# Kernel tuning notes

Hardware: AMD Instinct MI355X
Metric: run time of the kernel (lower is better)

The kernel has to match this reference:

```python
import jax, jax.numpy as jnp
import numpy as np

B, S, NB = 8, 512, 23
INIT, E, R, T = 512, 256, 3, 2
NEG = -9e8

def _gru(x, h, wih, whh, bih, bhh):
    gi = x @ wih.T + bih
    gh = h @ whh.T + bhh
    ir, iz, inn = jnp.split(gi, 3, axis=-1)
    hr, hz, hn = jnp.split(gh, 3, axis=-1)
    r = jax.nn.sigmoid(ir + hr)
    z = jax.nn.sigmoid(iz + hz)
    n = jnp.tanh(inn + r * hn)
    return (1.0 - z) * n + z * h

def setup_inputs():
    key = jax.random.key(0)
    ks = jax.random.split(key, 30)
    def lin(k, o, i):
        return jax.random.normal(k, (o, i), jnp.float32) * 0.02
    def vec(k, n):
        return jax.random.normal(k, (n,), jnp.float32) * 0.02
    inp = {}
    inp["amino_list"] = jax.random.normal(ks[0], (B, S, INIT), jnp.float32)
    inp["amino_mask"] = (jax.random.uniform(ks[1], (B, S)) < 0.9).astype(jnp.float32)
    inp["emb_W"] = lin(ks[2], E, INIT); inp["emb_b"] = vec(ks[3], E)
    inp["nb_W"] = lin(ks[4], E, INIT); inp["nb_b"] = vec(ks[5], E)
    inp["align_W"] = jax.random.normal(ks[6], (R, 1, 2 * E), jnp.float32) * 0.02
    inp["align_b"] = jax.random.normal(ks[7], (R, 1), jnp.float32) * 0.02
    inp["attend_W"] = jax.random.normal(ks[8], (R, E, E), jnp.float32) * 0.02
    inp["attend_b"] = jax.random.normal(ks[9], (R, E), jnp.float32) * 0.02
    inp["gru_wih"] = jax.random.normal(ks[10], (R, 3 * E, E), jnp.float32) * 0.02
    inp["gru_whh"] = jax.random.normal(ks[11], (R, 3 * E, E), jnp.float32) * 0.02
    inp["gru_bih"] = jax.random.normal(ks[12], (R, 3 * E), jnp.float32) * 0.02
    inp["gru_bhh"] = jax.random.normal(ks[13], (R, 3 * E), jnp.float32) * 0.02
    inp["seq_align_W"] = lin(ks[14], 1, 2 * E); inp["seq_align_b"] = vec(ks[15], 1)
    inp["seq_attend_W"] = lin(ks[16], E, E); inp["seq_attend_b"] = vec(ks[17], E)
    inp["seq_gru_wih"] = lin(ks[18], 3 * E, E); inp["seq_gru_bih"] = vec(ks[19], 3 * E)
    inp["seq_gru_whh"] = lin(ks[20], 3 * E, E); inp["seq_gru_bhh"] = vec(ks[21], 3 * E)
    inp["amino_degree_list"] = jax.random.randint(ks[22], (B, S, NB), -1, S)
    return inp

def reference(amino_list, amino_mask, emb_W, emb_b, nb_W, nb_b, align_W, align_b,
              attend_W, attend_b, gru_wih, gru_whh, gru_bih, gru_bhh,
              seq_align_W, seq_align_b, seq_attend_W, seq_attend_b,
              seq_gru_wih, seq_gru_whh, seq_gru_bih, seq_gru_bhh, amino_degree_list):
    idx = amino_degree_list
    lrelu = jax.nn.leaky_relu
    # per-batch neighbor gather: (S,D),(S,NB) -> (S,NB,D); index -1 wraps (masked out below)
    gather = jax.vmap(lambda f, i: f[i])
    feat = lrelu(amino_list @ emb_W.T + emb_b)               # (B,S,E)
    nfeat = lrelu(gather(amino_list, idx) @ nb_W.T + nb_b)   # (B,S,NB,E)
    attend_mask = (idx != -1).astype(feat.dtype)             # (B,S,NB)
    smask = jnp.where(idx == -1, NEG, 0.0).astype(feat.dtype)

    def attn(d, center, nbr):
        # align Linear on concat([center, nbr]) split into two matvecs (same math, no concat)
        aW = align_W[d, 0]
        score = lrelu(jnp.einsum('bse,e->bs', center, aW[:E])[:, :, None]
                      + jnp.einsum('bsne,e->bsn', nbr, aW[E:]) + align_b[d, 0])
        w = jax.nn.softmax(score + smask, axis=-1) * attend_mask   # softmax over neighbor axis
        nt = nbr @ attend_W[d].T + attend_b[d]
        return jax.nn.elu(jnp.einsum('bsn,bsne->bse', w, nt))

    h = _gru(attn(0, feat, nfeat).reshape(-1, E), feat.reshape(-1, E),
             gru_wih[0], gru_whh[0], gru_bih[0], gru_bhh[0])
    act = jax.nn.relu(h.reshape(B, S, E))
    for d in range(1, R):
        ctx = attn(d, act, gather(act, idx))
        h = _gru(ctx.reshape(-1, E), h, gru_wih[d], gru_whh[d], gru_bih[d], gru_bhh[d])
        act = jax.nn.relu(h.reshape(B, S, E))

    seq_feature = jnp.sum(act * amino_mask[:, :, None], axis=1)  # (B,E)
    act_mol = jax.nn.relu(seq_feature)                           # fixed across T (as in torch)
    seq_smask = jnp.where(amino_mask == 0, NEG, 0.0)
    saW = seq_align_W[0]
    act_seq = act_mol
    for _ in range(T):
        score = lrelu((act_mol @ saW[:E])[:, None]
                      + jnp.einsum('bse,e->bs', act, saW[E:]) + seq_align_b[0])
        w = jax.nn.softmax(score + seq_smask, axis=-1) * amino_mask  # softmax over seq axis
        tf = act @ seq_attend_W.T + seq_attend_b
        seq_ctx = jax.nn.elu(jnp.einsum('bs,bse->be', w, tf))
        seq_feature = _gru(seq_ctx, seq_feature, seq_gru_wih, seq_gru_whh, seq_gru_bih, seq_gru_bhh)
        act_seq = jax.nn.relu(seq_feature)
    return (act_seq, act)
```

## Files before the change

kernel.cpp:

```cpp
#include <hip/hip_runtime.h>
#include <math.h>


#define BSZ   8
#define SEQ   512
#define NBR   23
#define EMB   256
#define INITD 512
#define BS    (BSZ*SEQ)
#define G3    (3*EMB)
#define NEGV  -9e8f

typedef __attribute__((ext_vector_type(8))) short short8;
typedef __attribute__((ext_vector_type(4))) float f32x4;

__device__ __forceinline__ float lrelu(float x){ return x > 0.f ? x : 0.01f*x; }
__device__ __forceinline__ float elu1 (float x){ return x > 0.f ? x : (expf(x)-1.f); }
__device__ __forceinline__ float sigm (float x){ return 1.f/(1.f+expf(-x)); }
__device__ __forceinline__ float bf2f(ushort u){
    union { unsigned int i; float f; } v; v.i = ((unsigned int)u) << 16; return v.f;
}
__device__ __forceinline__ ushort f2bf(float f){
    union { float f; unsigned int i; } v; v.f = f;
    unsigned int u = v.i;
    return (ushort)((u + 0x7FFFu + ((u >> 16) & 1u)) >> 16);
}
__device__ __forceinline__ unsigned pk2(float a, float b){
    return (unsigned)f2bf(a) | ((unsigned)f2bf(b) << 16);
}
__device__ __forceinline__ void unpack8(uint4 v, float* o) {
    o[0]=bf2f((ushort)(v.x&0xffff)); o[1]=bf2f((ushort)(v.x>>16));
    o[2]=bf2f((ushort)(v.y&0xffff)); o[3]=bf2f((ushort)(v.y>>16));
    o[4]=bf2f((ushort)(v.z&0xffff)); o[5]=bf2f((ushort)(v.z>>16));
    o[6]=bf2f((ushort)(v.w&0xffff)); o[7]=bf2f((ushort)(v.w>>16));
}

__device__ __forceinline__ void gload_lds16(const void* g, void* l) {
    __builtin_amdgcn_global_load_lds(
        (const __attribute__((address_space(1))) unsigned int*)g,
        (__attribute__((address_space(3))) unsigned int*)l,
        16, 0, 0);
}

__global__ __launch_bounds__(256) void convert_flat(
    const float* __restrict__ amino, ushort* __restrict__ aminobf,
    const float* __restrict__ embW,  ushort* __restrict__ embWbf,
    const float* __restrict__ nbW,   ushort* __restrict__ nbWbf,
    const float* __restrict__ attW,  ushort* __restrict__ attWbf,
    const float* __restrict__ gwih,  ushort* __restrict__ gwihbf,
    const float* __restrict__ gwhh,  ushort* __restrict__ gwhhbf,
    const float* __restrict__ satW,  ushort* __restrict__ satWbf,
    const float* __restrict__ sgwih, ushort* __restrict__ sgwihbf,
    const float* __restrict__ sgwhh, ushort* __restrict__ sgwhhbf,
    float* __restrict__ zeroBase)
{
    const unsigned stride = gridDim.x * 256;
    for (unsigned u = blockIdx.x*256 + threadIdx.x; u < 525568u; u += stride) {
        const float* s; ushort* d; unsigned lu;
        if      (u < 262144u) { s=amino; d=aminobf; lu=u; }
        else if (u < 278528u) { s=embW;  d=embWbf;  lu=u-262144u; }
        else if (u < 294912u) { s=nbW;   d=nbWbf;   lu=u-278528u; }
        else if (u < 319488u) { s=attW;  d=attWbf;  lu=u-294912u; }
        else if (u < 393216u) { s=gwih;  d=gwihbf;  lu=u-319488u; }
        else if (u < 466944u) { s=gwhh;  d=gwhhbf;  lu=u-393216u; }
        else if (u < 475136u) { s=satW;  d=satWbf;  lu=u-466944u; }
        else if (u < 499712u) { s=sgwih; d=sgwihbf; lu=u-475136u; }
        else if (u < 524288u) { s=sgwhh; d=sgwhhbf; lu=u-499712u; }
        else {
            unsigned i = (u - 524288u) * 8;
            *reinterpret_cast<float4*>(&zeroBase[i])     = make_float4(0,0,0,0);
            *reinterpret_cast<float4*>(&zeroBase[i + 4]) = make_float4(0,0,0,0);
            continue;
        }
        size_t i = (size_t)lu * 8;
        float4 a = *reinterpret_cast<const float4*>(s + i);
        float4 b = *reinterpret_cast<const float4*>(s + i + 4);
        uint4 o;
        o.x = pk2(a.x, a.y); o.y = pk2(a.z, a.w);
        o.z = pk2(b.x, b.y); o.w = pk2(b.z, b.w);
        *reinterpret_cast<uint4*>(d + i) = o;
    }
}

struct GemmLds64 { ushort A[2][128][64]; ushort B[2][64][64]; };

template<int ACT, int DOTS>
__device__ __forceinline__ void gemm64_dev(
    const ushort* __restrict__ A, const ushort* __restrict__ W,
    const float* __restrict__ bias,
    float* __restrict__ C, ushort* __restrict__ Cbf,
    const float* __restrict__ dotW, float* __restrict__ dotOut,
    int N, int K, int bx, int by, GemmLds64& L)
{
    const int tid = threadIdx.x;
    const int m0 = bx * 128, n0 = by * 64;
    const int wv = tid >> 6, lane = tid & 63;
    const int fr = lane & 15, grp = lane >> 4;
    const int kc = K >> 3;
    const int mh = wv & 1, nh = wv >> 1;
    const int lrow = lane >> 3;
    const int csrc = (lane & 7) ^ lrow;

    f32x4 acc[4][2];
    #pragma unroll
    for (int i = 0; i < 4; ++i)
        #pragma unroll
        for (int n = 0; n < 2; ++n) acc[i][n] = (f32x4){0.f,0.f,0.f,0.f};

    auto stage = [&](int c, int k0) {
        const int kch = (k0 >> 3) + csrc;
        #pragma unroll
        for (int i = 0; i < 4; ++i) {
            const int s = (wv << 2) + i;
            gload_lds16(A + ((size_t)(m0 + (s << 3) + lrow) * kc + kch) * 8,
                        &L.A[c][s << 3][0]);
        }
        #pragma unroll
        for (int i = 0; i < 2; ++i) {
            const int s = (wv << 1) + i;
            gload_lds16(W + ((size_t)(n0 + (s << 3) + lrow) * kc + kch) * 8,
                        &L.B[c][s << 3][0]);
        }
    };
    auto compute = [&](int c) {
        #pragma unroll
        for (int ks = 0; ks < 2; ++ks) {
            short8 af[4];
            #pragma unroll
            for (int i = 0; i < 4; ++i) {
                const int ar = (mh << 6) + (i << 4) + fr;
                af[i] = *reinterpret_cast<const short8*>(
                    &L.A[c][ar][(((ks << 2) + grp) ^ (ar & 7)) << 3]);
            }
            #pragma unroll
            for (int n = 0; n < 2; ++n) {
                const int br = (nh << 5) + (n << 4) + fr;
                short8 bv = *reinterpret_cast<const short8*>(
                    &L.B[c][br][(((ks << 2) + grp) ^ (br & 7)) << 3]);
                #pragma unroll
                for (int i = 0; i < 4; ++i)
                    acc[i][n] = __builtin_amdgcn_mfma_f32_16x16x32_bf16(
                        af[i], bv, acc[i][n], 0, 0, 0);
            }
        }
    };

    const int KT = K >> 6;
    stage(0, 0);
    __syncthreads();
    int cur = 0;
    for (int kt = 1; kt < KT; ++kt) {
        stage(cur ^ 1, kt << 6);
        compute(cur);
        __syncthreads();
        cur ^= 1;
    }
    compute(cur);

    float pd[4][4];
    if (DOTS) {
        #pragma unroll
        for (int i = 0; i < 4; ++i)
            #pragma unroll
            for (int j = 0; j < 4; ++j) pd[i][j] = 0.f;
    }
    #pragma unroll
    for (int i = 0; i < 4; ++i) {
        const int mrow = m0 + (mh << 6) + (i << 4) + (grp << 2);
        #pragma unroll
        for (int n = 0; n < 2; ++n) {
            const int col = n0 + (nh << 5) + (n << 4) + fr;
            const float bv = bias[col];
            const float dw = DOTS ? dotW[col] : 0.f;
            #pragma unroll
            for (int j = 0; j < 4; ++j) {
                float t = acc[i][n][j] + bv;
                if (ACT == 1) t = lrelu(t);
                size_t off = (size_t)(mrow + j) * N + col;
                if (C)   C[off] = t;
                if (Cbf) Cbf[off] = f2bf(t);
                if (DOTS) pd[i][j] += t * dw;
            }
        }
    }
    if (DOTS) {
        #pragma unroll
        for (int i = 0; i < 4; ++i)
            #pragma unroll
            for (int j = 0; j < 4; ++j) {
                float v = pd[i][j];
                v += __shfl_xor(v, 1, 64);
                v += __shfl_xor(v, 2, 64);
                v += __shfl_xor(v, 4, 64);
                v += __shfl_xor(v, 8, 64);
                if (fr == 0)
                    atomicAdd(&dotOut[m0 + (mh << 6) + (i << 4) + (grp << 2) + j], v);
            }
    }
}

__global__ __launch_bounds__(256) void featnbase_kernel(
    const ushort* __restrict__ aminobf,
    const ushort* __restrict__ embWbf, const float* __restrict__ embB,
    ushort* __restrict__ featbf,
    const ushort* __restrict__ nbWbf, const float* __restrict__ nbB,
    ushort* __restrict__ nbasebf,
    const float* __restrict__ alignW,
    float* __restrict__ cdot, float* __restrict__ ndot)
{
    __shared__ GemmLds64 L;
    int blk = blockIdx.x;
    if (blk < 128)
        gemm64_dev<1,1>(aminobf, embWbf, embB, nullptr, featbf,
                        alignW, cdot, EMB, INITD, blk & 31, blk >> 5, L);
    else {
        blk -= 128;
        gemm64_dev<1,1>(aminobf, nbWbf, nbB, nullptr, nbasebf,
                        alignW + EMB, ndot, EMB, INITD, blk & 31, blk >> 5, L);
    }
}

struct GALds { ushort ctxpre[16][256]; ushort ctx[16][256]; float wsum_s[16]; };

__global__ __launch_bounds__(512) void gatherattend_kernel(
    const float* __restrict__ cdot, const float* __restrict__ ndot,
    const int* __restrict__ idx, const ushort* __restrict__ nbr,
    const float* __restrict__ alignBd,
    const ushort* __restrict__ attWd, const float* __restrict__ attBd,
    ushort* __restrict__ ctxbf)
{
    __shared__ GALds L;
    const int tid = threadIdx.x;
    const int r0 = blockIdx.x * 16;

    {
        const int row16 = tid >> 5, sub = tid & 31;
        const int r = r0 + row16, b = r >> 9;
        float sc = -3e38f, vm = 0.f; int rn = 0;
        if (sub < NBR) {
            int j = idx[(size_t)r*NBR + sub];
            int valid = (j >= 0);
            int jj = valid ? j : j + SEQ;
            rn = b*SEQ + jj;
            vm = (float)valid;
            sc = lrelu(cdot[r] + ndot[rn] + alignBd[0]) + (valid ? 0.f : NEGV);
        }
        float m = sc;
        #pragma unroll
        for (int off = 16; off; off >>= 1) m = fmaxf(m, __shfl_xor(m, off, 32));
        float ev = (sub < NBR) ? expf(sc - m) : 0.f;
        float s = ev;
        #pragma unroll
        for (int off = 16; off; off >>= 1) s += __shfl_xor(s, off, 32);
        float wgt = ev * vm / s;
        float ws = wgt;
        #pragma unroll
        for (int off = 16; off; off >>= 1) ws += __shfl_xor(ws, off, 32);
        float a8[8] = {};
        const int e0 = sub << 3;
        #pragma unroll
        for (int n = 0; n < NBR; ++n) {
            float wn = __shfl(wgt, n, 32);
            int   rr = __shfl(rn, n, 32);
            uint4 v = *reinterpret_cast<const uint4*>(&nbr[(size_t)rr*EMB + e0]);
            float x[8]; unpack8(v, x);
            #pragma unroll
            for (int i = 0; i < 8; ++i) a8[i] += wn * x[i];
        }
        uint4 o;
        o.x = pk2(a8[0],a8[1]); o.y = pk2(a8[2],a8[3]);
        o.z = pk2(a8[4],a8[5]); o.w = pk2(a8[6],a8[7]);
        *reinterpret_cast<uint4*>(&L.ctxpre[row16][(sub ^ (row16&7)) << 3]) = o;
        if (sub == 0) L.wsum_s[row16] = ws;
    }
    __syncthreads();

    const int wv = tid >> 6, lane = tid & 63;
    const int fr = lane & 15, grp = lane >> 4;
    {
        f32x4 acc[2] = {(f32x4){0,0,0,0},(f32x4){0,0,0,0}};
        #pragma unroll
        for (int kt = 0; kt < 8; ++kt) {
            short8 af = *reinterpret_cast<const short8*>(
                &L.ctxpre[fr][((((kt<<2)+grp) ^ (fr&7)) << 3)]);
            #pragma unroll
            for (int f = 0; f < 2; ++f) {
                const int col = (wv<<5) + (f<<4) + fr;
                short8 bv = *reinterpret_cast<const short8*>(
                    &attWd[(size_t)col*EMB + (kt<<5) + (grp<<3)]);
                acc[f] = __builtin_amdgcn_mfma_f32_16x16x32_bf16(af, bv, acc[f], 0, 0, 0);
            }
        }
        #pragma unroll
        for (int f = 0; f < 2; ++f) {
            const int col = (wv<<5) + (f<<4) + fr;
            const float bb = attBd[col];
            #pragma unroll
            for (int j = 0; j < 4; ++j) {
                const int row = (grp<<2) + j;
                L.ctx[row][col] = f2bf(elu1(acc[f][j] + L.wsum_s[row]*bb));
            }
        }
    }
    __syncthreads();
    {
        const int row = tid >> 5, c = tid & 31;
        uint4 v = *reinterpret_cast<const uint4*>(&L.ctx[row][c << 3]);
        *reinterpret_cast<uint4*>(&ctxbf[(size_t)(r0+row)*EMB + (c << 3)]) = v;
    }
}

__global__ __launch_bounds__(256) void gigh_kernel(
    const ushort* __restrict__ ctxbf, const ushort* __restrict__ gwihd,
    const float* __restrict__ gbihd, ushort* __restrict__ gibf,
    const ushort* __restrict__ hprevbf, const ushort* __restrict__ gwhhd,
    const float* __restrict__ gbhhd, ushort* __restrict__ ghbf)
{
    __shared__ GemmLds64 L;
    int blk = blockIdx.x;
    if (blk < 384)
        gemm64_dev<0,0>(ctxbf, gwihd, gbihd, nullptr, gibf, nullptr, nullptr,
                        G3, EMB, blk & 31, blk >> 5, L);
    else {
        blk -= 384;
        gemm64_dev<0,0>(hprevbf, gwhhd, gbhhd, nullptr, ghbf, nullptr, nullptr,
                        G3, EMB, blk & 31, blk >> 5, L);
    }
}

template<int LAST>
__global__ __launch_bounds__(512) void grudot_kernel(
    const ushort* __restrict__ gibf, const ushort* __restrict__ ghbf,
    const ushort* __restrict__ hprevbf, const float* __restrict__ nextW,
    const float* __restrict__ mask,
    ushort* __restrict__ hbf, float* __restrict__ actout,
    ushort* __restrict__ actbf,
    float* __restrict__ cdotO, float* __restrict__ ndotO,
    float* __restrict__ seqfeatA)
{
    __shared__ float sred[16][256];
    const int tid = threadIdx.x;
    const int row = tid >> 5, sub = tid & 31;
    const int e0 = sub << 3;
    const size_t r = (size_t)blockIdx.x * 16 + row;
    const size_t gb = r*G3;
    uint4 giA = *reinterpret_cast<const uint4*>(&gibf[gb + e0]);
    uint4 giB = *reinterpret_cast<const uint4*>(&gibf[gb + 256 + e0]);
    uint4 giC = *reinterpret_cast<const uint4*>(&gibf[gb + 512 + e0]);
    uint4 ghA = *reinterpret_cast<const uint4*>(&ghbf[gb + e0]);
    uint4 ghB = *reinterpret_cast<const uint4*>(&ghbf[gb + 256 + e0]);
    uint4 ghC = *reinterpret_cast<const uint4*>(&ghbf[gb + 512 + e0]);
    uint4 hpv = *reinterpret_cast<const uint4*>(&hprevbf[r*EMB + e0]);
    float ir_[8], iz_[8], in_[8], hr_[8], hz_[8], hn_[8], hp_[8];
    unpack8(giA, ir_); unpack8(giB, iz_); unpack8(giC, in_);
    unpack8(ghA, hr_); unpack8(ghB, hz_); unpack8(ghC, hn_);
    unpack8(hpv, hp_);
    float hv8[8], av8[8];
    #pragma unroll
    for (int i = 0; i < 8; ++i) {
        float rg = sigm(ir_[i] + hr_[i]);
        float z  = sigm(iz_[i] + hz_[i]);
        float n  = tanhf(in_[i] + rg*hn_[i]);
        hv8[i] = (1.f - z)*n + z*hp_[i];
        av8[i] = fmaxf(hv8[i], 0.f);
    }
    if (LAST) {
        *reinterpret_cast<float4*>(&actout[r*EMB + e0])     = make_float4(av8[0],av8[1],av8[2],av8[3]);
        *reinterpret_cast<float4*>(&actout[r*EMB + e0 + 4]) = make_float4(av8[4],av8[5],av8[6],av8[7]);
    }
    uint4 hb, ab;
    hb.x = pk2(hv8[0],hv8[1]); hb.y = pk2(hv8[2],hv8[3]);
    hb.z = pk2(hv8[4],hv8[5]); hb.w = pk2(hv8[6],hv8[7]);
    ab.x = pk2(av8[0],av8[1]); ab.y = pk2(av8[2],av8[3]);
    ab.z = pk2(av8[4],av8[5]); ab.w = pk2(av8[6],av8[7]);
    *reinterpret_cast<uint4*>(&hbf[r*EMB + e0])   = hb;
    *reinterpret_cast<uint4*>(&actbf[r*EMB + e0]) = ab;
    float pc = 0.f, pn = 0.f;
    float4 w1a = *reinterpret_cast<const float4*>(&nextW[EMB + e0]);
    float4 w1b = *reinterpret_cast<const float4*>(&nextW[EMB + e0 + 4]);
    pn = av8[0]*w1a.x + av8[1]*w1a.y + av8[2]*w1a.z + av8[3]*w1a.w
       + av8[4]*w1b.x + av8[5]*w1b.y + av8[6]*w1b.z + av8[7]*w1b.w;
    if (!LAST) {
        float4 w0a = *reinterpret_cast<const float4*>(&nextW[e0]);
        float4 w0b = *reinterpret_cast<const float4*>(&nextW[e0 + 4]);
        pc = av8[0]*w0a.x + av8[1]*w0a.y + av8[2]*w0a.z + av8[3]*w0a.w
           + av8[4]*w0b.x + av8[5]*w0b.y + av8[6]*w0b.z + av8[7]*w0b.w;
    }
    #pragma unroll
    for (int off = 16; off; off >>= 1) {
        pn += __shfl_xor(pn, off, 32);
        if (!LAST) pc += __shfl_xor(pc, off, 32);
    }
    if (sub == 0) {
        if (!LAST) cdotO[r] = pc;
        ndotO[r] = pn;
    }
    if (LAST) {
        const float mk = mask[r];
        #pragma unroll
        for (int i = 0; i < 8; ++i) sred[row][e0 + i] = av8[i] * mk;
        __syncthreads();
        if (tid < 256) {
            float s = 0.f;
            #pragma unroll
            for (int rr = 0; rr < 16; ++rr) s += sred[rr][tid];
            atomicAdd(&seqfeatA[(blockIdx.x >> 5)*EMB + tid], s);
        }
    }
}

__global__ __launch_bounds__(256) void seqpre_kernel(
    const ushort* __restrict__ actbf, const ushort* __restrict__ satWbf,
    const float* __restrict__ satB, float* __restrict__ tf)
{
    __shared__ GemmLds64 L;
    gemm64_dev<0,0>(actbf, satWbf, satB, tf, nullptr, nullptr, nullptr,
                    EMB, EMB, blockIdx.x & 31, blockIdx.x >> 5, L);
}

__global__ __launch_bounds__(256) void seqpv2_kernel(
    const float* __restrict__ ad, const float* __restrict__ mask,
    const float* __restrict__ saB, const float* __restrict__ saW,
    const float* __restrict__ seqfeat, const float* __restrict__ tf,
    float* __restrict__ partial)
{
    const int st = blockIdx.x, b = blockIdx.y;
    const int tid = threadIdx.x;
    __shared__ float w_s[SEQ];
    __shared__ float red[256];
    red[tid] = fmaxf(seqfeat[b*EMB + tid], 0.f) * saW[tid];
    __syncthreads();
    for (int off = 128; off; off >>= 1) {
        if (tid < off) red[tid] += red[tid + off];
        __syncthreads();
    }
    const float cb = red[0];
    __syncthreads();
    float mk0 = mask[b*SEQ + tid], mk1 = mask[b*SEQ + 256 + tid];
    float bb = saB[0];
    float s0 = lrelu(cb + ad[b*SEQ + tid] + bb)       + (mk0 == 0.f ? NEGV : 0.f);
    float s1 = lrelu(cb + ad[b*SEQ + 256 + tid] + bb) + (mk1 == 0.f ? NEGV : 0.f);
    red[tid] = fmaxf(s0, s1); __syncthreads();
    for (int off = 128; off; off >>= 1) {
        if (tid < off) red[tid] = fmaxf(red[tid], red[tid + off]);
        __syncthreads();
    }
    float m = red[0]; __syncthreads();
    float e0 = expf(s0 - m), e1 = expf(s1 - m);
    red[tid] = e0 + e1; __syncthreads();
    for (int off = 128; off; off >>= 1) {
        if (tid < off) red[tid] += red[tid + off];
        __syncthreads();
    }
    float inv = 1.f / red[0];
    w_s[tid]       = e0 * inv * mk0;
    w_s[tid + 256] = e1 * inv * mk1;
    __syncthreads();
    float acc = 0.f;
    const int s0i = st * 32;
    #pragma unroll 4
    for (int s = s0i; s < s0i + 32; ++s)
        acc += w_s[s] * tf[((size_t)b*SEQ + s)*EMB + tid];
    partial[((size_t)b*16 + st)*EMB + tid] = acc;
}

template<int T0>
__global__ __launch_bounds__(512) void seqstep_kernel(
    const float* __restrict__ partial, const float* __restrict__ sfin,
    const ushort* __restrict__ sgwihbf, const float* __restrict__ sgbih,
    const ushort* __restrict__ sgwhhbf, const float* __restrict__ sgbhh,
    float* __restrict__ sgi, float* __restrict__ sfout,
    float* __restrict__ actseq)
{
    const int b = blockIdx.x >> 2, q = blockIdx.x & 3;
    const int tid = threadIdx.x, lane = tid & 63, wv = tid >> 6;
    __shared__ float xs[EMB];
    __shared__ float hs[EMB];
    __shared__ float gis[192], ghs[192];
    if (tid < EMB) {
        hs[tid] = sfin[b*EMB + tid];
        if (T0) {
            float a = 0.f;
            #pragma unroll
            for (int st = 0; st < 16; ++st)
                a += partial[((size_t)b*16 + st)*EMB + tid];
            xs[tid] = elu1(a);
        }
    }
    if (!T0) {
        for (int l = tid; l < 192; l += 512) {
            int g = (l >> 6)*EMB + (q << 6) + (l & 63);
            gis[l] = sgi[b*G3 + g];
        }
    }
    __syncthreads();
    const int nrows = T0 ? 384 : 192;
    const int rpw = nrows >> 3;
    for (int i = 0; i < rpw; ++i) {
        const int l = wv * rpw + i;
        const int iswih = T0 && (l < 192);
        const int ll = (T0 && l >= 192) ? l - 192 : l;
        const int g = (ll >> 6)*EMB + (q << 6) + (ll & 63);
        const ushort* Wm = iswih ? sgwihbf : sgwhhbf;
        ushort4 w4 = *reinterpret_cast<const ushort4*>(&Wm[(size_t)g*EMB + (lane << 2)]);
        float4 x4 = *reinterpret_cast<const float4*>(iswih ? &xs[lane << 2] : &hs[lane << 2]);
        float d = bf2f(w4.x)*x4.x + bf2f(w4.y)*x4.y + bf2f(w4.z)*x4.z + bf2f(w4.w)*x4.w;
        #pragma unroll
        for (int off = 32; off; off >>= 1) d += __shfl_xor(d, off, 64);
        if (lane == 0) {
            if (iswih) {
                d += sgbih[g];
                gis[ll] = d;
                sgi[b*G3 + g] = d;
            } else {
                ghs[ll] = d + sgbhh[g];
            }
        }
    }
    __syncthreads();
    if (tid < 64) {
        const int e = (q << 6) + tid;
        float rg = sigm(gis[tid]       + ghs[tid]);
        float z  = sigm(gis[64 + tid]  + ghs[64 + tid]);
        float n  = tanhf(gis[128 + tid] + rg*ghs[128 + tid]);
        float hv = (1.f - z)*n + z*hs[e];
        sfout[b*EMB + e]  = hv;
        actseq[b*EMB + e] = fmaxf(hv, 0.f);
    }
}

extern "C" void kernel_launch(void* const* d_in, const int* in_sizes, int n_in,
                              void* d_out, int out_size, void* d_ws, size_t ws_size,
                              hipStream_t stream) {
    (void)in_sizes; (void)n_in; (void)out_size; (void)ws_size;
    const float* amino  = (const float*)d_in[0];
    const float* mask   = (const float*)d_in[1];
    const float* embW   = (const float*)d_in[2];
    const float* embB   = (const float*)d_in[3];
    const float* nbW    = (const float*)d_in[4];
    const float* nbB    = (const float*)d_in[5];
    const float* alignW = (const float*)d_in[6];
    const float* alignB = (const float*)d_in[7];
    const float* attW   = (const float*)d_in[8];
    const float* attB   = (const float*)d_in[9];
    const float* gwih   = (const float*)d_in[10];
    const float* gwhh   = (const float*)d_in[11];
    const float* gbih   = (const float*)d_in[12];
    const float* gbhh   = (const float*)d_in[13];
    const float* saW    = (const float*)d_in[14];
    const float* saB    = (const float*)d_in[15];
    const float* satW   = (const float*)d_in[16];
    const float* satB   = (const float*)d_in[17];
    const float* sgwih  = (const float*)d_in[18];
    const float* sgbih  = (const float*)d_in[19];
    const float* sgwhh  = (const float*)d_in[20];
    const float* sgbhh  = (const float*)d_in[21];
    const int*   idx    = (const int*)d_in[22];

    char* cur = (char*)d_ws;
    auto alloc = [&](size_t bytes) -> char* {
        char* p = cur; cur += (bytes + 255) & ~(size_t)255; return p;
    };
    float* seqfeat = (float*)alloc(BSZ*EMB*4);
    float* cdot    = (float*)alloc(BS*4);
    float* ndot    = (float*)alloc(BS*4);
    float* tf      = (float*)alloc((size_t)BS*EMB*4);
    float* sf2     = (float*)alloc(BSZ*EMB*4);
    float* sgi     = (float*)alloc(BSZ*G3*4);
    float* partial = (float*)alloc((size_t)BSZ*16*EMB*4);
    ushort* aminobf  = (ushort*)alloc((size_t)BS*INITD*2);
    ushort* featbf   = (ushort*)alloc((size_t)BS*EMB*2);
    ushort* nbasebf  = (ushort*)alloc((size_t)BS*EMB*2);
    ushort* actbf    = (ushort*)alloc((size_t)BS*EMB*2);
    ushort* hbf      = (ushort*)alloc((size_t)BS*EMB*2);
    ushort* ctxbf    = (ushort*)alloc((size_t)BS*EMB*2);
    ushort* gibf     = (ushort*)alloc((size_t)BS*G3*2);
    ushort* ghbf     = (ushort*)alloc((size_t)BS*G3*2);
    ushort* embWbf   = (ushort*)alloc((size_t)EMB*INITD*2);
    ushort* nbWbf    = (ushort*)alloc((size_t)EMB*INITD*2);
    ushort* attWbf   = (ushort*)alloc((size_t)3*EMB*EMB*2);
    ushort* gwihbf   = (ushort*)alloc((size_t)3*G3*EMB*2);
    ushort* gwhhbf   = (ushort*)alloc((size_t)3*G3*EMB*2);
    ushort* satWbf   = (ushort*)alloc((size_t)EMB*EMB*2);
    ushort* sgwihbf  = (ushort*)alloc((size_t)G3*EMB*2);
    ushort* sgwhhbf  = (ushort*)alloc((size_t)G3*EMB*2);

    float* out    = (float*)d_out;
    float* actseq = out;
    float* act    = out + BSZ*EMB;

    convert_flat<<<2048, 256, 0, stream>>>(
        amino, aminobf, embW, embWbf, nbW, nbWbf, attW, attWbf,
        gwih, gwihbf, gwhh, gwhhbf, satW, satWbf,
        sgwih, sgwihbf, sgwhh, sgwhhbf, seqfeat);

    featnbase_kernel<<<256, 256, 0, stream>>>(
        aminobf, embWbf, embB, featbf, nbWbf, nbB, nbasebf,
        alignW, cdot, ndot);

    for (int d = 0; d < 3; ++d) {
        const ushort* nbrbf   = (d == 0) ? nbasebf : actbf;
        const ushort* hprevbf = (d == 0) ? featbf  : hbf;
        gatherattend_kernel<<<BS/16, 512, 0, stream>>>(
            cdot, ndot, idx, nbrbf, alignB + d,
            attWbf + (size_t)d*EMB*EMB, attB + d*EMB, ctxbf);
        gigh_kernel<<<768, 256, 0, stream>>>(
            ctxbf, gwihbf + (size_t)d*G3*EMB, gbih + d*G3, gibf,
            hprevbf, gwhhbf + (size_t)d*G3*EMB, gbhh + d*G3, ghbf);
        if (d < 2) {
            grudot_kernel<0><<<BS/16, 512, 0, stream>>>(
                gibf, ghbf, hprevbf, alignW + (d+1)*2*EMB, mask,
                hbf, act, actbf, cdot, ndot, seqfeat);
        } else {
            grudot_kernel<1><<<BS/16, 512, 0, stream>>>(
                gibf, ghbf, hprevbf, saW, mask,
                hbf, act, actbf, cdot, ndot, seqfeat);
        }
    }

    seqpre_kernel<<<128, 256, 0, stream>>>(actbf, satWbf, satB, tf);
    seqpv2_kernel<<<dim3(16, BSZ), 256, 0, stream>>>(
        ndot, mask, saB, saW, seqfeat, tf, partial);
    seqstep_kernel<1><<<32, 512, 0, stream>>>(
        partial, seqfeat, sgwihbf, sgbih, sgwhhbf, sgbhh, sgi, sf2, actseq);
    seqstep_kernel<0><<<32, 512, 0, stream>>>(
        partial, sf2, sgwihbf, sgbih, sgwhhbf, sgbhh, sgi, seqfeat, actseq);
}
```

Measured before the change: 158.6 us.

## Overlap weight conversion with feature GEMM and fuse seq attend GEMM into pooling

The weight conversions not needed by the first GEMM move into extra blocks of the feature/neighbour GEMM kernel, so they run alongside it instead of in the leading convert pass. The separate seq-attend GEMM that wrote an fp32 tf buffer is folded into the softmax-pooling kernel. Each block now computes its 32-row tf tile with MFMA in LDS and reduces it directly, which removes a launch and the tf round trip through global memory. In exchange, each pooling block does more work, with B operands read straight from global memory and larger LDS use.

```diff
diff --git a/kernel.cpp b/kernel.cpp
--- a/kernel.cpp
+++ b/kernel.cpp
@@ -42,43 +42,51 @@
         16, 0, 0);
 }
 
-__global__ __launch_bounds__(256) void convert_flat(
+__device__ __forceinline__ void conv_unit(const float* s, ushort* d, size_t i) {
+    float4 a = *reinterpret_cast<const float4*>(s + i);
+    float4 b = *reinterpret_cast<const float4*>(s + i + 4);
+    uint4 o;
+    o.x = pk2(a.x, a.y); o.y = pk2(a.z, a.w);
+    o.z = pk2(b.x, b.y); o.w = pk2(b.z, b.w);
+    *reinterpret_cast<uint4*>(d + i) = o;
+}
+
+__global__ __launch_bounds__(256) void convert_core(
     const float* __restrict__ amino, ushort* __restrict__ aminobf,
     const float* __restrict__ embW,  ushort* __restrict__ embWbf,
     const float* __restrict__ nbW,   ushort* __restrict__ nbWbf,
-    const float* __restrict__ attW,  ushort* __restrict__ attWbf,
-    const float* __restrict__ gwih,  ushort* __restrict__ gwihbf,
-    const float* __restrict__ gwhh,  ushort* __restrict__ gwhhbf,
-    const float* __restrict__ satW,  ushort* __restrict__ satWbf,
-    const float* __restrict__ sgwih, ushort* __restrict__ sgwihbf,
-    const float* __restrict__ sgwhh, ushort* __restrict__ sgwhhbf,
     float* __restrict__ zeroBase)
 {
     const unsigned stride = gridDim.x * 256;
-    for (unsigned u = blockIdx.x*256 + threadIdx.x; u < 525568u; u += stride) {
-        const float* s; ushort* d; unsigned lu;
-        if      (u < 262144u) { s=amino; d=aminobf; lu=u; }
-        else if (u < 278528u) { s=embW;  d=embWbf;  lu=u-262144u; }
-        else if (u < 294912u) { s=nbW;   d=nbWbf;   lu=u-278528u; }
-        else if (u < 319488u) { s=attW;  d=attWbf;  lu=u-294912u; }
-        else if (u < 393216u) { s=gwih;  d=gwihbf;  lu=u-319488u; }
-        else if (u < 466944u) { s=gwhh;  d=gwhhbf;  lu=u-393216u; }
-        else if (u < 475136u) { s=satW;  d=satWbf;  lu=u-466944u; }
-        else if (u < 499712u) { s=sgwih; d=sgwihbf; lu=u-475136u; }
-        else if (u < 524288u) { s=sgwhh; d=sgwhhbf; lu=u-499712u; }
+    for (unsigned u = blockIdx.x*256 + threadIdx.x; u < 296192u; u += stride) {
+        if      (u < 262144u) conv_unit(amino, aminobf, (size_t)u*8);
+        else if (u < 278528u) conv_unit(embW,  embWbf,  (size_t)(u-262144u)*8);
+        else if (u < 294912u) conv_unit(nbW,   nbWbf,   (size_t)(u-278528u)*8);
         else {
-            unsigned i = (u - 524288u) * 8;
+            unsigned i = (u - 294912u) * 8;
             *reinterpret_cast<float4*>(&zeroBase[i])     = make_float4(0,0,0,0);
             *reinterpret_cast<float4*>(&zeroBase[i + 4]) = make_float4(0,0,0,0);
-            continue;
-        }
-        size_t i = (size_t)lu * 8;
-        float4 a = *reinterpret_cast<const float4*>(s + i);
-        float4 b = *reinterpret_cast<const float4*>(s + i + 4);
-        uint4 o;
-        o.x = pk2(a.x, a.y); o.y = pk2(a.z, a.w);
-        o.z = pk2(b.x, b.y); o.w = pk2(b.z, b.w);
-        *reinterpret_cast<uint4*>(d + i) = o;
+        }
+    }
+}
+
+__device__ __forceinline__ void convert_rest(
+    int blk, int nblk,
+    const float* attW, ushort* attWbf,
+    const float* gwih, ushort* gwihbf,
+    const float* gwhh, ushort* gwhhbf,
+    const float* satW, ushort* satWbf,
+    const float* sgwih, ushort* sgwihbf,
+    const float* sgwhh, ushort* sgwhhbf)
+{
+    const unsigned stride = nblk * 256;
+    for (unsigned u = blk*256 + threadIdx.x; u < 229376u; u += stride) {
+        if      (u < 24576u)  conv_unit(attW,  attWbf,  (size_t)u*8);
+        else if (u < 98304u)  conv_unit(gwih,  gwihbf,  (size_t)(u-24576u)*8);
+        else if (u < 172032u) conv_unit(gwhh,  gwhhbf,  (size_t)(u-98304u)*8);
+        else if (u < 180224u) conv_unit(satW,  satWbf,  (size_t)(u-172032u)*8);
+        else if (u < 204800u) conv_unit(sgwih, sgwihbf, (size_t)(u-180224u)*8);
+        else                  conv_unit(sgwhh, sgwhhbf, (size_t)(u-204800u)*8);
     }
 }
 
@@ -206,17 +214,26 @@
     const ushort* __restrict__ nbWbf, const float* __restrict__ nbB,
     ushort* __restrict__ nbasebf,
     const float* __restrict__ alignW,
-    float* __restrict__ cdot, float* __restrict__ ndot)
+    float* __restrict__ cdot, float* __restrict__ ndot,
+    const float* attW, ushort* attWbf,
+    const float* gwih, ushort* gwihbf,
+    const float* gwhh, ushort* gwhhbf,
+    const float* satW, ushort* satWbf,
+    const float* sgwih, ushort* sgwihbf,
+    const float* sgwhh, ushort* sgwhhbf)
 {
     __shared__ GemmLds64 L;
     int blk = blockIdx.x;
     if (blk < 128)
         gemm64_dev<1,1>(aminobf, embWbf, embB, nullptr, featbf,
                         alignW, cdot, EMB, INITD, blk & 31, blk >> 5, L);
-    else {
+    else if (blk < 256) {
         blk -= 128;
         gemm64_dev<1,1>(aminobf, nbWbf, nbB, nullptr, nbasebf,
                         alignW + EMB, ndot, EMB, INITD, blk & 31, blk >> 5, L);
+    } else {
+        convert_rest(blk - 256, 128, attW, attWbf, gwih, gwihbf,
+                     gwhh, gwhhbf, satW, satWbf, sgwih, sgwihbf, sgwhh, sgwhhbf);
     }
 }
 
@@ -409,25 +426,30 @@
     }
 }
 
-__global__ __launch_bounds__(256) void seqpre_kernel(
-    const ushort* __restrict__ actbf, const ushort* __restrict__ satWbf,
-    const float* __restrict__ satB, float* __restrict__ tf)
-{
-    __shared__ GemmLds64 L;
-    gemm64_dev<0,0>(actbf, satWbf, satB, tf, nullptr, nullptr, nullptr,
-                    EMB, EMB, blockIdx.x & 31, blockIdx.x >> 5, L);
-}
-
-__global__ __launch_bounds__(256) void seqpv2_kernel(
+__global__ __launch_bounds__(256) void seqpvtf_kernel(
     const float* __restrict__ ad, const float* __restrict__ mask,
     const float* __restrict__ saB, const float* __restrict__ saW,
-    const float* __restrict__ seqfeat, const float* __restrict__ tf,
+    const float* __restrict__ seqfeat,
+    const ushort* __restrict__ actbf, const ushort* __restrict__ satWbf,
+    const float* __restrict__ satB,
     float* __restrict__ partial)
 {
     const int st = blockIdx.x, b = blockIdx.y;
     const int tid = threadIdx.x;
+    __shared__ ushort As[32][256];
+    __shared__ float tf_s[32][256];
     __shared__ float w_s[SEQ];
     __shared__ float red[256];
+    const int r0 = b*SEQ + st*32;
+
+    {
+        #pragma unroll
+        for (int i = 0; i < 4; ++i) {
+            const int row = (tid >> 5) + i*8, c = tid & 31;
+            uint4 v = *reinterpret_cast<const uint4*>(&actbf[(size_t)(r0+row)*EMB + (c<<3)]);
+            *reinterpret_cast<uint4*>(&As[row][(c ^ (row&7)) << 3]) = v;
+        }
+    }
     red[tid] = fmaxf(seqfeat[b*EMB + tid], 0.f) * saW[tid];
     __syncthreads();
     for (int off = 128; off; off >>= 1) {
@@ -446,22 +468,65 @@
         __syncthreads();
     }
     float m = red[0]; __syncthreads();
-    float e0 = expf(s0 - m), e1 = expf(s1 - m);
-    red[tid] = e0 + e1; __syncthreads();
+    float e0v = expf(s0 - m), e1v = expf(s1 - m);
+    red[tid] = e0v + e1v; __syncthreads();
     for (int off = 128; off; off >>= 1) {
         if (tid < off) red[tid] += red[tid + off];
         __syncthreads();
     }
     float inv = 1.f / red[0];
-    w_s[tid]       = e0 * inv * mk0;
-    w_s[tid + 256] = e1 * inv * mk1;
-    __syncthreads();
-    float acc = 0.f;
-    const int s0i = st * 32;
-    #pragma unroll 4
-    for (int s = s0i; s < s0i + 32; ++s)
-        acc += w_s[s] * tf[((size_t)b*SEQ + s)*EMB + tid];
-    partial[((size_t)b*16 + st)*EMB + tid] = acc;
+    w_s[tid]       = e0v * inv * mk0;
+    w_s[tid + 256] = e1v * inv * mk1;
+    __syncthreads();
+
+    {
+        const int wv = tid >> 6, lane = tid & 63;
+        const int fr = lane & 15, grp = lane >> 4;
+        f32x4 acc[2][4];
+        #pragma unroll
+        for (int mt = 0; mt < 2; ++mt)
+            #pragma unroll
+            for (int f = 0; f < 4; ++f) acc[mt][f] = (f32x4){0,0,0,0};
+        #pragma unroll
+        for (int kt = 0; kt < 8; ++kt) {
+            short8 af[2];
+            #pragma unroll
+            for (int mt = 0; mt < 2; ++mt) {
+                const int ar = (mt << 4) + fr;
+                af[mt] = *reinterpret_cast<const short8*>(
+                    &As[ar][((((kt<<2)+grp) ^ (ar&7)) << 3)]);
+            }
+            #pragma unroll
+            for (int f = 0; f < 4; ++f) {
+                const int col = (wv<<6) + (f<<4) + fr;
+                short8 bv = *reinterpret_cast<const short8*>(
+                    &satWbf[(size_t)col*EMB + (kt<<5) + (grp<<3)]);
+                #pragma unroll
+                for (int mt = 0; mt < 2; ++mt)
+                    acc[mt][f] = __builtin_amdgcn_mfma_f32_16x16x32_bf16(
+                        af[mt], bv, acc[mt][f], 0, 0, 0);
+            }
+        }
+        #pragma unroll
+        for (int f = 0; f < 4; ++f) {
+            const int col = (wv<<6) + (f<<4) + fr;
+            const float bias = satB[col];
+            #pragma unroll
+            for (int mt = 0; mt < 2; ++mt)
+                #pragma unroll
+                for (int j = 0; j < 4; ++j)
+                    tf_s[(mt<<4) + (grp<<2) + j][col] = acc[mt][f][j] + bias;
+        }
+    }
+    __syncthreads();
+    {
+        float acc = 0.f;
+        const int s0i = st * 32;
+        #pragma unroll 4
+        for (int s = 0; s < 32; ++s)
+            acc += w_s[s0i + s] * tf_s[s][tid];
+        partial[((size_t)b*16 + st)*EMB + tid] = acc;
+    }
 }
 
 template<int T0>
@@ -564,7 +629,6 @@
     float* seqfeat = (float*)alloc(BSZ*EMB*4);
     float* cdot    = (float*)alloc(BS*4);
     float* ndot    = (float*)alloc(BS*4);
-    float* tf      = (float*)alloc((size_t)BS*EMB*4);
     float* sf2     = (float*)alloc(BSZ*EMB*4);
     float* sgi     = (float*)alloc(BSZ*G3*4);
     float* partial = (float*)alloc((size_t)BSZ*16*EMB*4);
@@ -589,14 +653,14 @@
     float* actseq = out;
     float* act    = out + BSZ*EMB;
 
-    convert_flat<<<2048, 256, 0, stream>>>(
-        amino, aminobf, embW, embWbf, nbW, nbWbf, attW, attWbf,
-        gwih, gwihbf, gwhh, gwhhbf, satW, satWbf,
-        sgwih, sgwihbf, sgwhh, sgwhhbf, seqfeat);
-
-    featnbase_kernel<<<256, 256, 0, stream>>>(
+    convert_core<<<1280, 256, 0, stream>>>(
+        amino, aminobf, embW, embWbf, nbW, nbWbf, seqfeat);
+
+    featnbase_kernel<<<384, 256, 0, stream>>>(
         aminobf, embWbf, embB, featbf, nbWbf, nbB, nbasebf,
-        alignW, cdot, ndot);
+        alignW, cdot, ndot,
+        attW, attWbf, gwih, gwihbf, gwhh, gwhhbf,
+        satW, satWbf, sgwih, sgwihbf, sgwhh, sgwhhbf);
 
     for (int d = 0; d < 3; ++d) {
         const ushort* nbrbf   = (d == 0) ? nbasebf : actbf;
@@ -618,9 +682,8 @@
         }
     }
 
-    seqpre_kernel<<<128, 256, 0, stream>>>(actbf, satWbf, satB, tf);
-    seqpv2_kernel<<<dim3(16, BSZ), 256, 0, stream>>>(
-        ndot, mask, saB, saW, seqfeat, tf, partial);
+    seqpvtf_kernel<<<dim3(16, BSZ), 256, 0, stream>>>(
+        ndot, mask, saB, saW, seqfeat, actbf, satWbf, satB, partial);
     seqstep_kernel<1><<<32, 512, 0, stream>>>(
         partial, seqfeat, sgwihbf, sgbih, sgwhhbf, sgbhh, sgi, sf2, actseq);
     seqstep_kernel<0><<<32, 512, 0, stream>>>(
```

Result: no change. 157.0 us, median of 2 (-1.0%).
